# Kernel optimization log

Hardware: AMD Instinct MI355X
Metric: run time of the kernel (lower is better)

## Reference

```python
import jax, jax.numpy as jnp
import numpy as np

T, B, D = 1024, 4, 1024  # seq_len, batch, d_model (module is seq-first: data[T,B,D])


def setup_inputs() -> dict:
    key = jax.random.key(0)
    ks = jax.random.split(key, 5)
    data = jax.random.normal(ks[0], (T, B, D), jnp.float32)
    # torch Linear equivalent: y = x @ W + b with W stored [in, out]
    W_qkv = jax.random.normal(ks[1], (D, 3 * D), jnp.float32) * 0.02
    b_qkv = jnp.zeros((3 * D,), jnp.float32)
    # Pos_bias param interpolated to [T,T]; with T == seq_len it's the raw param.
    pos_bias = jax.random.normal(ks[2], (T, T), jnp.float32) * 0.02
    W_out = jax.random.normal(ks[3], (D, D), jnp.float32) * 0.02
    b_out = jnp.zeros((D,), jnp.float32)
    return dict(data=data, W_qkv=W_qkv, b_qkv=b_qkv, pos_bias=pos_bias,
                W_out=W_out, b_out=b_out)


def reference(data, W_qkv, b_qkv, pos_bias, W_out, b_out):
    # layer_norm=False -> Identity; dropout unused in forward
    qkv = data @ W_qkv + b_qkv                 # [T,B,3D]
    q, k, v = jnp.split(qkv, 3, axis=-1)       # each [T,B,D]
    P = jnp.exp(pos_bias)                      # [T,T], exp of (identity-interpolated) pos bias
    ek = jnp.exp(k)                            # [T,B,D]
    # einsum 'ijb,jbd->ibd' with b==1 broadcast on pos_bias == 'tj,jbd->tbd'
    num = jnp.einsum('tj,jbd->tbd', P, ek * v)  # [T,B,D]
    den = jnp.einsum('tj,jbd->tbd', P, ek)      # [T,B,D]
    out = jax.nn.sigmoid(q) * (num / den)       # gated AFT output
    return out @ W_out + b_out                  # [T,B,D]
```

## Files before the change

kernel.cpp:

```cpp
#include <hip/hip_runtime.h>
#include <hip/hip_bf16.h>
#include <cstdint>
#include <cstddef>


typedef __bf16 bf16_t;
typedef __attribute__((ext_vector_type(8))) __bf16 bf16x8;
typedef __attribute__((ext_vector_type(4))) __bf16 bf16x4;
typedef __attribute__((ext_vector_type(4))) float floatx4;

#define T_DIM 1024
#define B_DIM 4
#define D_DIM 1024
#define R_DIM (T_DIM * B_DIM)
#define N_QKV (3 * D_DIM)
#define N_ND  (2 * R_DIM)

__global__ void k_cvt(const float* __restrict__ in, bf16_t* __restrict__ out,
                      int n, int do_exp) {
    int i = (blockIdx.x * blockDim.x + threadIdx.x) * 4;
    if (i >= n) return;
    float4 v = *reinterpret_cast<const float4*>(in + i);
    bf16x4 o;
    if (do_exp) {
        o[0] = (bf16_t)__expf(v.x); o[1] = (bf16_t)__expf(v.y);
        o[2] = (bf16_t)__expf(v.z); o[3] = (bf16_t)__expf(v.w);
    } else {
        o[0] = (bf16_t)v.x; o[1] = (bf16_t)v.y;
        o[2] = (bf16_t)v.z; o[3] = (bf16_t)v.w;
    }
    *reinterpret_cast<bf16x4*>(out + i) = o;
}

__global__ void k_tconv(const float* __restrict__ in, bf16_t* __restrict__ out,
                        int K, int N) {
    __shared__ float s[32][33];
    int n0 = blockIdx.x * 32, k0 = blockIdx.y * 32;
    int tx = threadIdx.x & 31, ty = threadIdx.x >> 5;
#pragma unroll
    for (int i = 0; i < 4; ++i)
        s[ty + i * 8][tx] = in[(size_t)(k0 + ty + i * 8) * N + n0 + tx];
    __syncthreads();
#pragma unroll
    for (int i = 0; i < 4; ++i)
        out[(size_t)(n0 + ty + i * 8) * K + k0 + tx] = (bf16_t)s[tx][ty + i * 8];
}

__global__ void k_e1(const float* __restrict__ qkv, bf16_t* __restrict__ BndT) {
    __shared__ float sk[32][33], sv[32][33];
    int j0 = blockIdx.x * 32, d0 = blockIdx.y * 32, b = blockIdx.z;
    int tx = threadIdx.x & 31, ty = threadIdx.x >> 5;
#pragma unroll
    for (int i = 0; i < 4; ++i) {
        int j = j0 + ty + i * 8;
        size_t base = (size_t)j * (B_DIM * N_QKV) + (size_t)b * N_QKV;
        float kk = qkv[base + D_DIM + d0 + tx];
        float vv = qkv[base + 2 * D_DIM + d0 + tx];
        float e = __expf(kk);
        sk[ty + i * 8][tx] = e;
        sv[ty + i * 8][tx] = e * vv;
    }
    __syncthreads();
#pragma unroll
    for (int i = 0; i < 4; ++i) {
        int d = d0 + ty + i * 8;
        int r = b * D_DIM + d;
        BndT[(size_t)r * T_DIM + j0 + tx] = (bf16_t)sv[tx][ty + i * 8];
        BndT[(size_t)(R_DIM + r) * T_DIM + j0 + tx] = (bf16_t)sk[tx][ty + i * 8];
    }
}

__global__ void k_e2(const float* __restrict__ qkv, const float* __restrict__ Cnd,
                     bf16_t* __restrict__ Y) {
    int idx = (blockIdx.x * blockDim.x + threadIdx.x) * 4;
    int d = idx & (D_DIM - 1);
    int b = (idx >> 10) & 3;
    int t = idx >> 12;
    float4 q   = *reinterpret_cast<const float4*>(
        qkv + (size_t)t * (B_DIM * N_QKV) + (size_t)b * N_QKV + d);
    float4 num = *reinterpret_cast<const float4*>(
        Cnd + (size_t)t * N_ND + b * D_DIM + d);
    float4 den = *reinterpret_cast<const float4*>(
        Cnd + (size_t)t * N_ND + R_DIM + b * D_DIM + d);
    bf16x4 o;
    o[0] = (bf16_t)(num.x / (den.x * (1.0f + __expf(-q.x))));
    o[1] = (bf16_t)(num.y / (den.y * (1.0f + __expf(-q.y))));
    o[2] = (bf16_t)(num.z / (den.z * (1.0f + __expf(-q.z))));
    o[3] = (bf16_t)(num.w / (den.w * (1.0f + __expf(-q.w))));
    *reinterpret_cast<bf16x4*>(Y + idx) = o;
}

__global__ __launch_bounds__(256)
void k_gemm(const bf16_t* __restrict__ A, const bf16_t* __restrict__ BT,
            const float* __restrict__ bias, float* __restrict__ C,
            int M, int N, int K) {
    __shared__ __align__(16) bf16_t As[128 * 32];
    __shared__ __align__(16) bf16_t Bs[128 * 32];
    const int tid = threadIdx.x;
    const int wid = tid >> 6, lane = tid & 63;
    const int wm = wid >> 1, wn = wid & 1;
    const int row0 = blockIdx.x * 128, col0 = blockIdx.y * 128;

    floatx4 acc[4][4];
#pragma unroll
    for (int m = 0; m < 4; ++m)
#pragma unroll
        for (int n = 0; n < 4; ++n) acc[m][n] = (floatx4){0.f, 0.f, 0.f, 0.f};

    const int lr = lane & 15;
    const int kq = (lane >> 4) * 8;

    const int e0 = wid * 1024 + lane * 8;
    const int ra0 = e0 >> 5, kk0 = e0 & 31;
    const int ra1 = (e0 + 512) >> 5, kk1 = (e0 + 512) & 31;

    const bf16_t* Ab = A + (size_t)row0 * K;
    const bf16_t* Bb = BT + (size_t)col0 * K;

    for (int kt = 0; kt < K; kt += 32) {
        __syncthreads();
        __builtin_amdgcn_global_load_lds(
            (const __attribute__((address_space(1))) void*)(Ab + (size_t)ra0 * K + kt + kk0),
            (__attribute__((address_space(3))) void*)(As + wid * 1024), 16, 0, 0);
        __builtin_amdgcn_global_load_lds(
            (const __attribute__((address_space(1))) void*)(Ab + (size_t)ra1 * K + kt + kk1),
            (__attribute__((address_space(3))) void*)(As + wid * 1024 + 512), 16, 0, 0);
        __builtin_amdgcn_global_load_lds(
            (const __attribute__((address_space(1))) void*)(Bb + (size_t)ra0 * K + kt + kk0),
            (__attribute__((address_space(3))) void*)(Bs + wid * 1024), 16, 0, 0);
        __builtin_amdgcn_global_load_lds(
            (const __attribute__((address_space(1))) void*)(Bb + (size_t)ra1 * K + kt + kk1),
            (__attribute__((address_space(3))) void*)(Bs + wid * 1024 + 512), 16, 0, 0);
        __syncthreads();

        bf16x8 af[4], bfr[4];
#pragma unroll
        for (int m = 0; m < 4; ++m)
            af[m] = *reinterpret_cast<const bf16x8*>(As + (wm * 64 + m * 16 + lr) * 32 + kq);
#pragma unroll
        for (int n = 0; n < 4; ++n)
            bfr[n] = *reinterpret_cast<const bf16x8*>(Bs + (wn * 64 + n * 16 + lr) * 32 + kq);
#pragma unroll
        for (int m = 0; m < 4; ++m)
#pragma unroll
            for (int n = 0; n < 4; ++n)
                acc[m][n] = __builtin_amdgcn_mfma_f32_16x16x32_bf16(af[m], bfr[n], acc[m][n], 0, 0, 0);
    }

    const int lg = lane >> 4;
#pragma unroll
    for (int n = 0; n < 4; ++n) {
        int col = col0 + wn * 64 + n * 16 + lr;
        float bv = bias ? bias[col] : 0.0f;
#pragma unroll
        for (int m = 0; m < 4; ++m) {
            int row = row0 + wm * 64 + m * 16 + lg * 4;
            float* Cp = C + (size_t)row * N + col;
#pragma unroll
            for (int j = 0; j < 4; ++j) Cp[(size_t)j * N] = acc[m][n][j] + bv;
        }
    }
}

extern "C" void kernel_launch(void* const* d_in, const int* in_sizes, int n_in,
                              void* d_out, int out_size, void* d_ws, size_t ws_size,
                              hipStream_t stream) {
    const float* data     = (const float*)d_in[0];
    const float* W_qkv    = (const float*)d_in[1];
    const float* b_qkv    = (const float*)d_in[2];
    const float* pos_bias = (const float*)d_in[3];
    const float* W_out    = (const float*)d_in[4];
    const float* b_out    = (const float*)d_in[5];
    float* out = (float*)d_out;

    char* ws = (char*)d_ws;
    const size_t MB = 1024 * 1024;
    bf16_t* data_bf = (bf16_t*)(ws + 0);
    bf16_t* WqkvT   = (bf16_t*)(ws + 8 * MB);
    bf16_t* WoutT   = (bf16_t*)(ws + 14 * MB);
    bf16_t* P_bf    = (bf16_t*)(ws + 16 * MB);
    float*  qkv     = (float*) (ws + 18 * MB);
    bf16_t* BndT    = (bf16_t*)(ws + 66 * MB);
    float*  Cnd     = (float*) (ws + 82 * MB);
    bf16_t* Y       = (bf16_t*)(ws + 0);

    k_cvt<<<dim3(R_DIM * D_DIM / 1024), dim3(256), 0, stream>>>(data, data_bf, R_DIM * D_DIM, 0);
    k_cvt<<<dim3(T_DIM * T_DIM / 1024), dim3(256), 0, stream>>>(pos_bias, P_bf, T_DIM * T_DIM, 1);
    k_tconv<<<dim3(N_QKV / 32, D_DIM / 32), dim3(256), 0, stream>>>(W_qkv, WqkvT, D_DIM, N_QKV);
    k_tconv<<<dim3(D_DIM / 32, D_DIM / 32), dim3(256), 0, stream>>>(W_out, WoutT, D_DIM, D_DIM);
    k_gemm<<<dim3(R_DIM / 128, N_QKV / 128), dim3(256), 0, stream>>>(
        data_bf, WqkvT, b_qkv, qkv, R_DIM, N_QKV, D_DIM);
    k_e1<<<dim3(T_DIM / 32, D_DIM / 32, B_DIM), dim3(256), 0, stream>>>(qkv, BndT);
    k_gemm<<<dim3(T_DIM / 128, N_ND / 128), dim3(256), 0, stream>>>(
        P_bf, BndT, nullptr, Cnd, T_DIM, N_ND, T_DIM);
    k_e2<<<dim3(R_DIM * D_DIM / 1024), dim3(256), 0, stream>>>(qkv, Cnd, Y);
    k_gemm<<<dim3(R_DIM / 128, D_DIM / 128), dim3(256), 0, stream>>>(
        Y, WoutT, b_out, out, R_DIM, D_DIM, D_DIM);
}
```

Measured before the change: 209.1 us.

## Fuse sigmoid-gate and num/den division into the positional-bias GEMM epilogue

Interleaves the exp(k)*v and exp(k) rows of the positional GEMM's B operand in 16-row groups, so each wave holds matching numerator and denominator tiles in registers. The GEMM epilogue then applies the sigmoid gate and division and writes bf16 Y directly. This removes the fp32 Cnd intermediate (a 32 MB write and re-read) and the separate elementwise kernel launch. In exchange, the epilogue stores are strided bf16 scalar writes and the q reads are uncoalesced.

```diff
diff --git a/kernel.cpp b/kernel.cpp
--- a/kernel.cpp
+++ b/kernel.cpp
@@ -65,29 +65,10 @@
     for (int i = 0; i < 4; ++i) {
         int d = d0 + ty + i * 8;
         int r = b * D_DIM + d;
-        BndT[(size_t)r * T_DIM + j0 + tx] = (bf16_t)sv[tx][ty + i * 8];
-        BndT[(size_t)(R_DIM + r) * T_DIM + j0 + tx] = (bf16_t)sk[tx][ty + i * 8];
-    }
-}
-
-__global__ void k_e2(const float* __restrict__ qkv, const float* __restrict__ Cnd,
-                     bf16_t* __restrict__ Y) {
-    int idx = (blockIdx.x * blockDim.x + threadIdx.x) * 4;
-    int d = idx & (D_DIM - 1);
-    int b = (idx >> 10) & 3;
-    int t = idx >> 12;
-    float4 q   = *reinterpret_cast<const float4*>(
-        qkv + (size_t)t * (B_DIM * N_QKV) + (size_t)b * N_QKV + d);
-    float4 num = *reinterpret_cast<const float4*>(
-        Cnd + (size_t)t * N_ND + b * D_DIM + d);
-    float4 den = *reinterpret_cast<const float4*>(
-        Cnd + (size_t)t * N_ND + R_DIM + b * D_DIM + d);
-    bf16x4 o;
-    o[0] = (bf16_t)(num.x / (den.x * (1.0f + __expf(-q.x))));
-    o[1] = (bf16_t)(num.y / (den.y * (1.0f + __expf(-q.y))));
-    o[2] = (bf16_t)(num.z / (den.z * (1.0f + __expf(-q.z))));
-    o[3] = (bf16_t)(num.w / (den.w * (1.0f + __expf(-q.w))));
-    *reinterpret_cast<bf16x4*>(Y + idx) = o;
+        int rr = ((r >> 4) << 5) + (r & 15);
+        BndT[(size_t)rr * T_DIM + j0 + tx] = (bf16_t)sv[tx][ty + i * 8];
+        BndT[(size_t)(rr + 16) * T_DIM + j0 + tx] = (bf16_t)sk[tx][ty + i * 8];
+    }
 }
 
 __global__ __launch_bounds__(256)
@@ -162,6 +143,86 @@
     }
 }
 
+__global__ __launch_bounds__(256)
+void k_gemm_aft(const bf16_t* __restrict__ A, const bf16_t* __restrict__ BT,
+                const float* __restrict__ qkv, bf16_t* __restrict__ Y) {
+    const int M = T_DIM, N = N_ND, K = T_DIM;
+    (void)M; (void)N;
+    __shared__ __align__(16) bf16_t As[128 * 32];
+    __shared__ __align__(16) bf16_t Bs[128 * 32];
+    const int tid = threadIdx.x;
+    const int wid = tid >> 6, lane = tid & 63;
+    const int wm = wid >> 1, wn = wid & 1;
+    const int row0 = blockIdx.x * 128, col0 = blockIdx.y * 128;
+
+    floatx4 acc[4][4];
+#pragma unroll
+    for (int m = 0; m < 4; ++m)
+#pragma unroll
+        for (int n = 0; n < 4; ++n) acc[m][n] = (floatx4){0.f, 0.f, 0.f, 0.f};
+
+    const int lr = lane & 15;
+    const int kq = (lane >> 4) * 8;
+
+    const int e0 = wid * 1024 + lane * 8;
+    const int ra0 = e0 >> 5, kk0 = e0 & 31;
+    const int ra1 = (e0 + 512) >> 5, kk1 = (e0 + 512) & 31;
+
+    const bf16_t* Ab = A + (size_t)row0 * K;
+    const bf16_t* Bb = BT + (size_t)col0 * K;
+
+    for (int kt = 0; kt < K; kt += 32) {
+        __syncthreads();
+        __builtin_amdgcn_global_load_lds(
+            (const __attribute__((address_space(1))) void*)(Ab + (size_t)ra0 * K + kt + kk0),
+            (__attribute__((address_space(3))) void*)(As + wid * 1024), 16, 0, 0);
+        __builtin_amdgcn_global_load_lds(
+            (const __attribute__((address_space(1))) void*)(Ab + (size_t)ra1 * K + kt + kk1),
+            (__attribute__((address_space(3))) void*)(As + wid * 1024 + 512), 16, 0, 0);
+        __builtin_amdgcn_global_load_lds(
+            (const __attribute__((address_space(1))) void*)(Bb + (size_t)ra0 * K + kt + kk0),
+            (__attribute__((address_space(3))) void*)(Bs + wid * 1024), 16, 0, 0);
+        __builtin_amdgcn_global_load_lds(
+            (const __attribute__((address_space(1))) void*)(Bb + (size_t)ra1 * K + kt + kk1),
+            (__attribute__((address_space(3))) void*)(Bs + wid * 1024 + 512), 16, 0, 0);
+        __syncthreads();
+
+        bf16x8 af[4], bfr[4];
+#pragma unroll
+        for (int m = 0; m < 4; ++m)
+            af[m] = *reinterpret_cast<const bf16x8*>(As + (wm * 64 + m * 16 + lr) * 32 + kq);
+#pragma unroll
+        for (int n = 0; n < 4; ++n)
+            bfr[n] = *reinterpret_cast<const bf16x8*>(Bs + (wn * 64 + n * 16 + lr) * 32 + kq);
+#pragma unroll
+        for (int m = 0; m < 4; ++m)
+#pragma unroll
+            for (int n = 0; n < 4; ++n)
+                acc[m][n] = __builtin_amdgcn_mfma_f32_16x16x32_bf16(af[m], bfr[n], acc[m][n], 0, 0, 0);
+    }
+
+    const int lg = lane >> 4;
+#pragma unroll
+    for (int p = 0; p < 2; ++p) {
+        int ncol = col0 + wn * 64 + p * 32 + lr;
+        int r = ((ncol >> 5) << 4) + lr;
+        int b = r >> 10, d = r & (D_DIM - 1);
+#pragma unroll
+        for (int m = 0; m < 4; ++m) {
+            int trow = row0 + wm * 64 + m * 16 + lg * 4;
+#pragma unroll
+            for (int j = 0; j < 4; ++j) {
+                int t = trow + j;
+                float num = acc[m][2 * p][j];
+                float den = acc[m][2 * p + 1][j];
+                float q = qkv[(size_t)t * (B_DIM * N_QKV) + (size_t)b * N_QKV + d];
+                float y = num / (den * (1.0f + __expf(-q)));
+                Y[(size_t)t * R_DIM + r] = (bf16_t)y;
+            }
+        }
+    }
+}
+
 extern "C" void kernel_launch(void* const* d_in, const int* in_sizes, int n_in,
                               void* d_out, int out_size, void* d_ws, size_t ws_size,
                               hipStream_t stream) {
@@ -181,7 +242,6 @@
     bf16_t* P_bf    = (bf16_t*)(ws + 16 * MB);
     float*  qkv     = (float*) (ws + 18 * MB);
     bf16_t* BndT    = (bf16_t*)(ws + 66 * MB);
-    float*  Cnd     = (float*) (ws + 82 * MB);
     bf16_t* Y       = (bf16_t*)(ws + 0);
 
     k_cvt<<<dim3(R_DIM * D_DIM / 1024), dim3(256), 0, stream>>>(data, data_bf, R_DIM * D_DIM, 0);
@@ -191,9 +251,8 @@
     k_gemm<<<dim3(R_DIM / 128, N_QKV / 128), dim3(256), 0, stream>>>(
         data_bf, WqkvT, b_qkv, qkv, R_DIM, N_QKV, D_DIM);
     k_e1<<<dim3(T_DIM / 32, D_DIM / 32, B_DIM), dim3(256), 0, stream>>>(qkv, BndT);
-    k_gemm<<<dim3(T_DIM / 128, N_ND / 128), dim3(256), 0, stream>>>(
-        P_bf, BndT, nullptr, Cnd, T_DIM, N_ND, T_DIM);
-    k_e2<<<dim3(R_DIM * D_DIM / 1024), dim3(256), 0, stream>>>(qkv, Cnd, Y);
+    k_gemm_aft<<<dim3(T_DIM / 128, N_ND / 128), dim3(256), 0, stream>>>(
+        P_bf, BndT, qkv, Y);
     k_gemm<<<dim3(R_DIM / 128, D_DIM / 128), dim3(256), 0, stream>>>(
         Y, WoutT, b_out, out, R_DIM, D_DIM, D_DIM);
 }
```

Result: faster. 193.9 us (-7.3%).
